# Performance work log

Hardware: AMD Instinct MI355X
Metric: run time of the kernel (lower is better)

## Reference

```python
import jax, jax.numpy as jnp
import numpy as np

BN_EPS = 1e-5

def setup_inputs() -> dict:
    key = jax.random.key(0)
    ks = jax.random.split(key, 6)
    B, C, H, W, Hd = 16, 512, 64, 64, 128
    return {
        "x": jax.random.normal(ks[0], (B, C, H, W), dtype=jnp.float32),
        "wA": jax.random.normal(ks[1], (Hd, C), dtype=jnp.float32) * 0.05,
        "wB": jax.random.normal(ks[2], (Hd, C), dtype=jnp.float32) * 0.05,
        "wC": jax.random.normal(ks[3], (Hd, C), dtype=jnp.float32) * 0.05,
        "wProj": jax.random.normal(ks[4], (C, Hd), dtype=jnp.float32) * 0.05,
        "bn_gamma": jnp.ones((C,), dtype=jnp.float32),
        "bn_beta": jnp.zeros((C,), dtype=jnp.float32),
        "bn_mean": jnp.zeros((C,), dtype=jnp.float32),
        "bn_var": jnp.ones((C,), dtype=jnp.float32),
    }

def reference(x, wA, wB, wC, wProj, bn_gamma, bn_beta, bn_mean, bn_var):
    B, C, H, W = x.shape
    N = H * W
    xf = x.reshape(B, C, N)                                  # [B, C, N]
    # three 1x1 convs (bias-free) == channel-mixing matmuls
    A = jax.nn.softmax(jnp.einsum('hc,bcn->bhn', wA, xf), axis=2)   # [B, Hd, N]
    Bf = jnp.einsum('hc,bcn->bhn', wB, xf)                          # [B, Hd, N]
    Cs = jax.nn.softmax(jnp.einsum('hc,bcn->bhn', wC, xf), axis=2)  # [B, Hd, N]
    # FeatureGathering = B_feat @ A^T : [B, Hd, Hd]
    G = jnp.einsum('bhn,bgn->bhg', Bf, A)
    # distribute: G @ C_softmax -> [B, Hd, N]
    y = jnp.einsum('bhg,bgn->bhn', G, Cs)
    # projection back to C channels + inference-mode BatchNorm
    p = jnp.einsum('ch,bhn->bcn', wProj, y)                         # [B, C, N]
    inv = jax.lax.rsqrt(bn_var + BN_EPS)
    out = (p - bn_mean[None, :, None]) * (inv * bn_gamma)[None, :, None] + bn_beta[None, :, None]
    return out.reshape(B, C, H, W)
```

## Files before the change

### kernel.cpp

```cpp
#include <hip/hip_runtime.h>
#include <cstddef>

#define NPIX 4096
#define CDIM 512

typedef _Float16 half8  __attribute__((ext_vector_type(8)));
typedef _Float16 half4v __attribute__((ext_vector_type(4)));
typedef float    f32x4  __attribute__((ext_vector_type(4)));

__device__ __forceinline__ void gl_lds16(const void* g, void* l) {
    __builtin_amdgcn_global_load_lds(
        (const __attribute__((address_space(1))) void*)g,
        (__attribute__((address_space(3))) void*)l, 16, 0, 0);
}

__global__ __launch_bounds__(256)
void prep(const float* __restrict__ wA, const float* __restrict__ wB,
          const float* __restrict__ wC, const float* __restrict__ wProj,
          _Float16* __restrict__ Wh, _Float16* __restrict__ WpH)
{
    if (blockIdx.x < 96) {
        const int gid  = blockIdx.x * 256 + threadIdx.x;
        const int lane = gid & 63;
        const int frag = gid >> 6;
        const int msub = frag & 7, kt = (frag >> 3) & 15, mt = frag >> 7;
        const float* __restrict__ W = (mt == 0) ? wA : (mt == 1) ? wB : wC;
        const int m  = msub * 16 + (lane & 15);
        const int c0 = kt * 32 + ((lane >> 4) << 3);
        const float* src = W + m * CDIM + c0;
        union { _Float16 h[8]; float4 f; } u;
#pragma unroll
        for (int j = 0; j < 8; ++j) u.h[j] = (_Float16)src[j];
        *(float4*)(Wh + (size_t)frag * 512 + lane * 8) = u.f;
    } else {
        const int gid = (blockIdx.x - 96) * 256 + threadIdx.x;
        const int i8  = gid * 8;
        float4 a = *(const float4*)(wProj + i8);
        float4 b = *(const float4*)(wProj + i8 + 4);
        union { _Float16 h[8]; float4 f; } u;
        u.h[0]=(_Float16)a.x; u.h[1]=(_Float16)a.y; u.h[2]=(_Float16)a.z; u.h[3]=(_Float16)a.w;
        u.h[4]=(_Float16)b.x; u.h[5]=(_Float16)b.y; u.h[6]=(_Float16)b.z; u.h[7]=(_Float16)b.w;
        *(float4*)(WpH + i8) = u.f;
    }
}

__global__ __launch_bounds__(256)
void conv_mfma(const float* __restrict__ x, const _Float16* __restrict__ Wh,
               _Float16* __restrict__ P)
{
    const int nt = blockIdx.x, mt = blockIdx.y, b = blockIdx.z;
    const int tid  = threadIdx.x;
    const int wave = tid >> 6, lane = tid & 63;
    const int wm = wave >> 1, wn = wave & 1;

    __shared__ alignas(16) _Float16 sA[4096];
    __shared__ alignas(16) _Float16 sB[128 * 40];

    f32x4 acc[4][4];
#pragma unroll
    for (int i = 0; i < 4; ++i)
#pragma unroll
        for (int j = 0; j < 4; ++j)
#pragma unroll
            for (int e = 0; e < 4; ++e) acc[i][j][e] = 0.f;

    const int n0 = (tid & 31) << 2;
    const int k0 = (tid >> 5) << 2;
    const float* xb = x + ((size_t)b << 21) + (nt << 7) + n0;
    const _Float16* WhB = Wh + (size_t)mt * 128 * 512;

    for (int kt = 0; kt < 16; ++kt) {
#pragma unroll
        for (int s = 0; s < 2; ++s) {
            const int frag = wave + (s << 2);
            gl_lds16(WhB + ((size_t)kt * 8 + frag) * 512 + lane * 8, &sA[frag * 512]);
        }
        const float* xs = xb + (size_t)(kt * 32 + k0) * NPIX;
        float ld[4][4];
        *(float4*)&ld[0][0] = *(const float4*)(xs);
        *(float4*)&ld[1][0] = *(const float4*)(xs + NPIX);
        *(float4*)&ld[2][0] = *(const float4*)(xs + 2 * NPIX);
        *(float4*)&ld[3][0] = *(const float4*)(xs + 3 * NPIX);
#pragma unroll
        for (int c = 0; c < 4; ++c) {
            const int n    = n0 + c;
            const int blkh = ((k0 >> 2) ^ (((n >> 4) & 3) << 1)) << 2;
            union { _Float16 h[4]; float2 f; } u;
            u.h[0] = (_Float16)ld[0][c];
            u.h[1] = (_Float16)ld[1][c];
            u.h[2] = (_Float16)ld[2][c];
            u.h[3] = (_Float16)ld[3][c];
            *(float2*)&sB[n * 40 + blkh] = u.f;
        }
        __syncthreads();

        half8 av[4], bv[4];
#pragma unroll
        for (int i = 0; i < 4; ++i)
            av[i] = *(const half8*)&sA[(((wm << 2) + i) << 9) + (lane << 3)];
#pragma unroll
        for (int j = 0; j < 4; ++j) {
            const int nj = (wn << 6) + (j << 4) + (lane & 15);
            const int qs = ((lane >> 4) ^ ((nj >> 4) & 3)) << 3;
            bv[j] = *(const half8*)&sB[nj * 40 + qs];
        }
#pragma unroll
        for (int i = 0; i < 4; ++i)
#pragma unroll
            for (int j = 0; j < 4; ++j)
                acc[i][j] = __builtin_amdgcn_mfma_f32_16x16x32_f16(bv[j], av[i], acc[i][j], 0, 0, 0);
        __syncthreads();
    }

    _Float16* Pb = P + (((size_t)b * 384 + mt * 128) << 12);
#pragma unroll
    for (int i = 0; i < 4; ++i) {
        const int m = (wm << 6) + (i << 4) + (lane & 15);
        _Float16* prow = Pb + (size_t)m * NPIX + (nt << 7) + (wn << 6) + ((lane >> 4) << 2);
#pragma unroll
        for (int j = 0; j < 4; ++j) {
            union { _Float16 h[4]; float2 f; } u;
#pragma unroll
            for (int r = 0; r < 4; ++r) u.h[r] = (_Float16)acc[i][j][r];
            *(float2*)(prow + (j << 4)) = u.f;
        }
    }
}

__global__ __launch_bounds__(256)
void softmax_rows(_Float16* __restrict__ P)
{
    const int blk = blockIdx.x;
    const int b   = blk >> 8;
    const int r   = blk & 255;
    const int m   = (r < 128) ? r : (r + 128);
    _Float16* row = P + (((size_t)b * 384 + m) << 12);
    const int tid = threadIdx.x;

    half8 h[2];
    float v[16];
    h[0] = *(const half8*)(row + tid * 16);
    h[1] = *(const half8*)(row + tid * 16 + 8);
    float mx = -3.402823466e38f;
#pragma unroll
    for (int j = 0; j < 16; ++j) { v[j] = (float)h[j >> 3][j & 7]; mx = fmaxf(mx, v[j]); }
#pragma unroll
    for (int o = 32; o > 0; o >>= 1) mx = fmaxf(mx, __shfl_xor(mx, o));
    __shared__ float redm[4];
    __shared__ float reds[4];
    const int wid = tid >> 6, lane = tid & 63;
    if (lane == 0) redm[wid] = mx;
    __syncthreads();
    mx = fmaxf(fmaxf(redm[0], redm[1]), fmaxf(redm[2], redm[3]));

    float s = 0.f;
#pragma unroll
    for (int j = 0; j < 16; ++j) { v[j] = __expf(v[j] - mx); s += v[j]; }
#pragma unroll
    for (int o = 32; o > 0; o >>= 1) s += __shfl_xor(s, o);
    if (lane == 0) reds[wid] = s;
    __syncthreads();
    s = (reds[0] + reds[1]) + (reds[2] + reds[3]);
    const float inv = 1.f / s;
#pragma unroll
    for (int j = 0; j < 16; ++j) h[j >> 3][j & 7] = (_Float16)(v[j] * inv);
    *(half8*)(row + tid * 16)     = h[0];
    *(half8*)(row + tid * 16 + 8) = h[1];
}

__global__ __launch_bounds__(256)
void g_partial_mfma(const _Float16* __restrict__ P, float* __restrict__ Gp)
{
    const int kc = blockIdx.x, b = blockIdx.y;
    const int tid  = threadIdx.x;
    const int wave = tid >> 6, lane = tid & 63;
    const int wm = wave >> 1, wn = wave & 1;

    const _Float16* Pa = P + ((size_t)b * 384 << 12);
    const _Float16* Pf = Pa + ((size_t)128 << 12);

    f32x4 acc[4][4];
#pragma unroll
    for (int i = 0; i < 4; ++i)
#pragma unroll
        for (int j = 0; j < 4; ++j)
#pragma unroll
            for (int e = 0; e < 4; ++e) acc[i][j][e] = 0.f;

    const int klane = ((lane >> 4) << 3);
    const int rlane = lane & 15;
#pragma unroll 2
    for (int kt = 0; kt < 8; ++kt) {
        const int k = (kc << 8) + (kt << 5) + klane;
        half8 av[4], bv[4];
#pragma unroll
        for (int i = 0; i < 4; ++i)
            av[i] = *(const half8*)(Pa + ((size_t)((wm << 6) + (i << 4) + rlane) << 12) + k);
#pragma unroll
        for (int j = 0; j < 4; ++j)
            bv[j] = *(const half8*)(Pf + ((size_t)((wn << 6) + (j << 4) + rlane) << 12) + k);
#pragma unroll
        for (int i = 0; i < 4; ++i)
#pragma unroll
            for (int j = 0; j < 4; ++j)
                acc[i][j] = __builtin_amdgcn_mfma_f32_16x16x32_f16(bv[j], av[i], acc[i][j], 0, 0, 0);
    }

    float* O = Gp + (((size_t)b * 16 + kc) << 14);
#pragma unroll
    for (int i = 0; i < 4; ++i) {
        const int g = (wm << 6) + (i << 4) + rlane;
        float* orow = O + (size_t)g * 128 + (wn << 6) + ((lane >> 4) << 2);
#pragma unroll
        for (int j = 0; j < 4; ++j)
            *(f32x4*)(orow + (j << 4)) = acc[i][j];
    }
}

__global__ __launch_bounds__(256)
void g_reduce_cvt(const float* __restrict__ Gp, _Float16* __restrict__ Gt)
{
    const int gid  = blockIdx.x * 256 + threadIdx.x;
    const int i8   = gid * 8;
    const int b    = i8 >> 14;
    const int rr   = i8 & 16383;
    const float* base = Gp + ((size_t)b << 18) + rr;
    float s[8];
#pragma unroll
    for (int e = 0; e < 8; ++e) s[e] = 0.f;
#pragma unroll
    for (int kc = 0; kc < 16; ++kc) {
        float4 v0 = *(const float4*)(base + ((size_t)kc << 14));
        float4 v1 = *(const float4*)(base + ((size_t)kc << 14) + 4);
        s[0]+=v0.x; s[1]+=v0.y; s[2]+=v0.z; s[3]+=v0.w;
        s[4]+=v1.x; s[5]+=v1.y; s[6]+=v1.z; s[7]+=v1.w;
    }
    union { _Float16 h[8]; float4 f; } u;
#pragma unroll
    for (int e = 0; e < 8; ++e) u.h[e] = (_Float16)s[e];
    *(float4*)(Gt + ((size_t)b << 14) + rr) = u.f;
}

__global__ __launch_bounds__(256)
void proj_mfma(const _Float16* __restrict__ WpH, const _Float16* __restrict__ Gt,
               _Float16* __restrict__ Mh)
{
    const int ct = blockIdx.x, b = blockIdx.y;
    const int tid  = threadIdx.x;
    const int wave = tid >> 6, lane = tid & 63;
    const int wm = wave >> 1, wn = wave & 1;

    f32x4 acc[4][4];
#pragma unroll
    for (int i = 0; i < 4; ++i)
#pragma unroll
        for (int j = 0; j < 4; ++j)
#pragma unroll
            for (int e = 0; e < 4; ++e) acc[i][j][e] = 0.f;

    const int klane = ((lane >> 4) << 3);
    const int rlane = lane & 15;
    const _Float16* Gb = Gt + ((size_t)b << 14);
#pragma unroll
    for (int kt = 0; kt < 4; ++kt) {
        const int k = (kt << 5) + klane;
        half8 av[4], bv[4];
#pragma unroll
        for (int i = 0; i < 4; ++i)
            av[i] = *(const half8*)(WpH + (size_t)((ct << 7) + (wm << 6) + (i << 4) + rlane) * 128 + k);
#pragma unroll
        for (int j = 0; j < 4; ++j)
            bv[j] = *(const half8*)(Gb + (size_t)((wn << 6) + (j << 4) + rlane) * 128 + k);
#pragma unroll
        for (int i = 0; i < 4; ++i)
#pragma unroll
            for (int j = 0; j < 4; ++j)
                acc[i][j] = __builtin_amdgcn_mfma_f32_16x16x32_f16(bv[j], av[i], acc[i][j], 0, 0, 0);
    }

    _Float16* Mb = Mh + ((size_t)b << 16);
#pragma unroll
    for (int i = 0; i < 4; ++i) {
        const int c = (ct << 7) + (wm << 6) + (i << 4) + rlane;
        _Float16* mrow = Mb + (size_t)c * 128 + (wn << 6) + ((lane >> 4) << 2);
#pragma unroll
        for (int j = 0; j < 4; ++j) {
            union { _Float16 h[4]; float2 f; } u;
#pragma unroll
            for (int r = 0; r < 4; ++r) u.h[r] = (_Float16)acc[i][j][r];
            *(float2*)(mrow + (j << 4)) = u.f;
        }
    }
}

__global__ __launch_bounds__(256)
void final_mfma(const _Float16* __restrict__ P, const _Float16* __restrict__ Mh,
                const float* __restrict__ gamma, const float* __restrict__ beta,
                const float* __restrict__ mean,  const float* __restrict__ var,
                float* __restrict__ out)
{
    const int nt = blockIdx.x, ct = blockIdx.y, b = blockIdx.z;
    const int tid  = threadIdx.x;
    const int wave = tid >> 6, lane = tid & 63;
    const int wm = wave >> 1, wn = wave & 1;

    __shared__ alignas(16) _Float16 sB[128 * 40];

    f32x4 acc[4][4];
#pragma unroll
    for (int i = 0; i < 4; ++i)
#pragma unroll
        for (int j = 0; j < 4; ++j)
#pragma unroll
            for (int e = 0; e < 4; ++e) acc[i][j][e] = 0.f;

    const int n0 = (tid & 31) << 2;
    const int k0 = (tid >> 5) << 2;
    const int klane = ((lane >> 4) << 3);
    const int rlane = lane & 15;
    const _Float16* Cs  = P + (((size_t)b * 384 + 256) << 12) + (nt << 7) + n0;
    const _Float16* MhB = Mh + ((size_t)b << 16) + ((size_t)(ct << 7) << 7);

    for (int kt = 0; kt < 4; ++kt) {
        const _Float16* cs = Cs + ((size_t)((kt << 5) + k0) << 12);
        half4v ld0 = *(const half4v*)(cs);
        half4v ld1 = *(const half4v*)(cs + NPIX);
        half4v ld2 = *(const half4v*)(cs + 2 * NPIX);
        half4v ld3 = *(const half4v*)(cs + 3 * NPIX);
#pragma unroll
        for (int c = 0; c < 4; ++c) {
            const int n    = n0 + c;
            const int blkh = ((k0 >> 2) ^ (((n >> 4) & 3) << 1)) << 2;
            half4v col = { ld0[c], ld1[c], ld2[c], ld3[c] };
            *(half4v*)&sB[n * 40 + blkh] = col;
        }
        __syncthreads();

        half8 av[4], bv[4];
#pragma unroll
        for (int i = 0; i < 4; ++i)
            av[i] = *(const half8*)(MhB + (size_t)((wm << 6) + (i << 4) + rlane) * 128 + (kt << 5) + klane);
#pragma unroll
        for (int j = 0; j < 4; ++j) {
            const int nj = (wn << 6) + (j << 4) + rlane;
            const int qs = ((lane >> 4) ^ ((nj >> 4) & 3)) << 3;
            bv[j] = *(const half8*)&sB[nj * 40 + qs];
        }
#pragma unroll
        for (int i = 0; i < 4; ++i)
#pragma unroll
            for (int j = 0; j < 4; ++j)
                acc[i][j] = __builtin_amdgcn_mfma_f32_16x16x32_f16(bv[j], av[i], acc[i][j], 0, 0, 0);
        __syncthreads();
    }

    float* ob = out + ((size_t)b << 21);
#pragma unroll
    for (int i = 0; i < 4; ++i) {
        const int c   = (ct << 7) + (wm << 6) + (i << 4) + rlane;
        const float s = gamma[c] * rsqrtf(var[c] + 1e-5f);
        const float t = fmaf(-mean[c], s, beta[c]);
        float* row = ob + ((size_t)c << 12) + (nt << 7) + (wn << 6) + ((lane >> 4) << 2);
#pragma unroll
        for (int j = 0; j < 4; ++j) {
            f32x4 v;
#pragma unroll
            for (int r = 0; r < 4; ++r) v[r] = fmaf(acc[i][j][r], s, t);
            *(f32x4*)(row + (j << 4)) = v;
        }
    }
}

extern "C" void kernel_launch(void* const* d_in, const int* in_sizes, int n_in,
                              void* d_out, int out_size, void* d_ws, size_t ws_size,
                              hipStream_t stream)
{
    const float* x     = (const float*)d_in[0];
    const float* wA    = (const float*)d_in[1];
    const float* wB    = (const float*)d_in[2];
    const float* wC    = (const float*)d_in[3];
    const float* wProj = (const float*)d_in[4];
    const float* gamma = (const float*)d_in[5];
    const float* beta  = (const float*)d_in[6];
    const float* mean  = (const float*)d_in[7];
    const float* var   = (const float*)d_in[8];
    float* out = (float*)d_out;

    char* ws = (char*)d_ws;
    _Float16* P   = (_Float16*)(ws);
    float*    Gp  = (float*)(ws + 50331648);
    _Float16* Gt  = (_Float16*)(ws + 67108864);
    _Float16* WpH = (_Float16*)(ws + 67633152);
    _Float16* Mh  = (_Float16*)(ws + 67764224);
    _Float16* Wh  = (_Float16*)(ws + 69861376);

    prep          <<<dim3(128),       256, 0, stream>>>(wA, wB, wC, wProj, Wh, WpH);
    conv_mfma     <<<dim3(32, 3, 16), 256, 0, stream>>>(x, Wh, P);
    softmax_rows  <<<dim3(4096),      256, 0, stream>>>(P);
    g_partial_mfma<<<dim3(16, 16),    256, 0, stream>>>(P, Gp);
    g_reduce_cvt  <<<dim3(128),       256, 0, stream>>>(Gp, Gt);
    proj_mfma     <<<dim3(4, 16),     256, 0, stream>>>(WpH, Gt, Mh);
    final_mfma    <<<dim3(32, 4, 16), 256, 0, stream>>>(P, Mh, gamma, beta, mean, var, out);
}
```

Measured before the change: 324.3 us.

## Merge conv M-tiles into one block and reuse staged C tile across output channels

conv_mfma now launches 768-thread blocks that cover all three 128-row weight tiles, so each x tile is loaded from global and converted to fp16 once instead of three times. final_mfma stages the whole 128x128 Cs tile in LDS once and loops over the four output-channel tiles inside the block, which removes the repeated Cs reads and the per-k-step barriers. The cost is fewer, larger blocks: the grid drops from 1536 to 512 blocks in conv and from 2048 to 512 in final, with more LDS per block, which may lower occupancy and latency hiding. In conv, only 256 of the 768 threads do the x load work, so the other waves sit idle at the barrier.

```diff
diff --git a/kernel.cpp b/kernel.cpp
--- a/kernel.cpp
+++ b/kernel.cpp
@@ -44,16 +44,18 @@
     }
 }
 
-__global__ __launch_bounds__(256)
+__global__ __launch_bounds__(768)
 void conv_mfma(const float* __restrict__ x, const _Float16* __restrict__ Wh,
                _Float16* __restrict__ P)
 {
-    const int nt = blockIdx.x, mt = blockIdx.y, b = blockIdx.z;
+    const int nt = blockIdx.x, b = blockIdx.y;
     const int tid  = threadIdx.x;
     const int wave = tid >> 6, lane = tid & 63;
-    const int wm = wave >> 1, wn = wave & 1;
-
-    __shared__ alignas(16) _Float16 sA[4096];
+    const int mt = wave >> 2;
+    const int q  = wave & 3;
+    const int wm = q >> 1, wn = q & 1;
+
+    __shared__ alignas(16) _Float16 sA[3 * 8 * 512];
     __shared__ alignas(16) _Float16 sB[128 * 40];
 
     f32x4 acc[4][4];
@@ -64,46 +66,48 @@
 #pragma unroll
             for (int e = 0; e < 4; ++e) acc[i][j][e] = 0.f;
 
-    const int n0 = (tid & 31) << 2;
-    const int k0 = (tid >> 5) << 2;
-    const float* xb = x + ((size_t)b << 21) + (nt << 7) + n0;
-    const _Float16* WhB = Wh + (size_t)mt * 128 * 512;
-
     for (int kt = 0; kt < 16; ++kt) {
 #pragma unroll
         for (int s = 0; s < 2; ++s) {
-            const int frag = wave + (s << 2);
-            gl_lds16(WhB + ((size_t)kt * 8 + frag) * 512 + lane * 8, &sA[frag * 512]);
-        }
-        const float* xs = xb + (size_t)(kt * 32 + k0) * NPIX;
-        float ld[4][4];
-        *(float4*)&ld[0][0] = *(const float4*)(xs);
-        *(float4*)&ld[1][0] = *(const float4*)(xs + NPIX);
-        *(float4*)&ld[2][0] = *(const float4*)(xs + 2 * NPIX);
-        *(float4*)&ld[3][0] = *(const float4*)(xs + 3 * NPIX);
-#pragma unroll
-        for (int c = 0; c < 4; ++c) {
-            const int n    = n0 + c;
-            const int blkh = ((k0 >> 2) ^ (((n >> 4) & 3) << 1)) << 2;
-            union { _Float16 h[4]; float2 f; } u;
-            u.h[0] = (_Float16)ld[0][c];
-            u.h[1] = (_Float16)ld[1][c];
-            u.h[2] = (_Float16)ld[2][c];
-            u.h[3] = (_Float16)ld[3][c];
-            *(float2*)&sB[n * 40 + blkh] = u.f;
+            const int f    = wave * 2 + s;
+            const int fmt  = f >> 3, fsub = f & 7;
+            gl_lds16(Wh + (((size_t)fmt * 128) + kt * 8 + fsub) * 512 + lane * 8,
+                     &sA[f * 512]);
+        }
+        if (tid < 256) {
+            const int n0 = (tid & 31) << 2;
+            const int k0 = (tid >> 5) << 2;
+            const float* xs = x + ((size_t)b << 21) + (nt << 7) + n0
+                                + (size_t)(kt * 32 + k0) * NPIX;
+            float ld[4][4];
+            *(float4*)&ld[0][0] = *(const float4*)(xs);
+            *(float4*)&ld[1][0] = *(const float4*)(xs + NPIX);
+            *(float4*)&ld[2][0] = *(const float4*)(xs + 2 * NPIX);
+            *(float4*)&ld[3][0] = *(const float4*)(xs + 3 * NPIX);
+#pragma unroll
+            for (int c = 0; c < 4; ++c) {
+                const int n    = n0 + c;
+                const int blkh = ((k0 >> 2) ^ (((n >> 4) & 3) << 1)) << 2;
+                union { _Float16 h[4]; float2 f; } u;
+                u.h[0] = (_Float16)ld[0][c];
+                u.h[1] = (_Float16)ld[1][c];
+                u.h[2] = (_Float16)ld[2][c];
+                u.h[3] = (_Float16)ld[3][c];
+                *(float2*)&sB[n * 40 + blkh] = u.f;
+            }
         }
         __syncthreads();
 
         half8 av[4], bv[4];
-#pragma unroll
-        for (int i = 0; i < 4; ++i)
-            av[i] = *(const half8*)&sA[(((wm << 2) + i) << 9) + (lane << 3)];
 #pragma unroll
         for (int j = 0; j < 4; ++j) {
             const int nj = (wn << 6) + (j << 4) + (lane & 15);
             const int qs = ((lane >> 4) ^ ((nj >> 4) & 3)) << 3;
             bv[j] = *(const half8*)&sB[nj * 40 + qs];
         }
+#pragma unroll
+        for (int i = 0; i < 4; ++i)
+            av[i] = *(const half8*)&sA[(((mt << 3) + (wm << 2) + i) << 9) + (lane << 3)];
 #pragma unroll
         for (int i = 0; i < 4; ++i)
 #pragma unroll
@@ -299,28 +303,20 @@
                 const float* __restrict__ mean,  const float* __restrict__ var,
                 float* __restrict__ out)
 {
-    const int nt = blockIdx.x, ct = blockIdx.y, b = blockIdx.z;
+    const int nt = blockIdx.x, b = blockIdx.y;
     const int tid  = threadIdx.x;
     const int wave = tid >> 6, lane = tid & 63;
     const int wm = wave >> 1, wn = wave & 1;
 
-    __shared__ alignas(16) _Float16 sB[128 * 40];
-
-    f32x4 acc[4][4];
-#pragma unroll
-    for (int i = 0; i < 4; ++i)
-#pragma unroll
-        for (int j = 0; j < 4; ++j)
-#pragma unroll
-            for (int e = 0; e < 4; ++e) acc[i][j][e] = 0.f;
+    __shared__ alignas(16) _Float16 sB[4][128 * 40];
 
     const int n0 = (tid & 31) << 2;
     const int k0 = (tid >> 5) << 2;
     const int klane = ((lane >> 4) << 3);
     const int rlane = lane & 15;
-    const _Float16* Cs  = P + (((size_t)b * 384 + 256) << 12) + (nt << 7) + n0;
-    const _Float16* MhB = Mh + ((size_t)b << 16) + ((size_t)(ct << 7) << 7);
-
+    const _Float16* Cs = P + (((size_t)b * 384 + 256) << 12) + (nt << 7) + n0;
+
+#pragma unroll
     for (int kt = 0; kt < 4; ++kt) {
         const _Float16* cs = Cs + ((size_t)((kt << 5) + k0) << 12);
         half4v ld0 = *(const half4v*)(cs);
@@ -332,41 +328,56 @@
             const int n    = n0 + c;
             const int blkh = ((k0 >> 2) ^ (((n >> 4) & 3) << 1)) << 2;
             half4v col = { ld0[c], ld1[c], ld2[c], ld3[c] };
-            *(half4v*)&sB[n * 40 + blkh] = col;
-        }
-        __syncthreads();
-
-        half8 av[4], bv[4];
-#pragma unroll
-        for (int i = 0; i < 4; ++i)
-            av[i] = *(const half8*)(MhB + (size_t)((wm << 6) + (i << 4) + rlane) * 128 + (kt << 5) + klane);
-#pragma unroll
-        for (int j = 0; j < 4; ++j) {
-            const int nj = (wn << 6) + (j << 4) + rlane;
-            const int qs = ((lane >> 4) ^ ((nj >> 4) & 3)) << 3;
-            bv[j] = *(const half8*)&sB[nj * 40 + qs];
-        }
+            *(half4v*)&sB[kt][n * 40 + blkh] = col;
+        }
+    }
+    __syncthreads();
+
+    const _Float16* Mb = Mh + ((size_t)b << 16);
+    float* ob = out + ((size_t)b << 21);
+
+    for (int ct = 0; ct < 4; ++ct) {
+        f32x4 acc[4][4];
 #pragma unroll
         for (int i = 0; i < 4; ++i)
 #pragma unroll
             for (int j = 0; j < 4; ++j)
-                acc[i][j] = __builtin_amdgcn_mfma_f32_16x16x32_f16(bv[j], av[i], acc[i][j], 0, 0, 0);
-        __syncthreads();
-    }
-
-    float* ob = out + ((size_t)b << 21);
-#pragma unroll
-    for (int i = 0; i < 4; ++i) {
-        const int c   = (ct << 7) + (wm << 6) + (i << 4) + rlane;
-        const float s = gamma[c] * rsqrtf(var[c] + 1e-5f);
-        const float t = fmaf(-mean[c], s, beta[c]);
-        float* row = ob + ((size_t)c << 12) + (nt << 7) + (wn << 6) + ((lane >> 4) << 2);
-#pragma unroll
-        for (int j = 0; j < 4; ++j) {
-            f32x4 v;
-#pragma unroll
-            for (int r = 0; r < 4; ++r) v[r] = fmaf(acc[i][j][r], s, t);
-            *(f32x4*)(row + (j << 4)) = v;
+#pragma unroll
+                for (int e = 0; e < 4; ++e) acc[i][j][e] = 0.f;
+
+#pragma unroll
+        for (int kt = 0; kt < 4; ++kt) {
+            half8 av[4], bv[4];
+#pragma unroll
+            for (int i = 0; i < 4; ++i)
+                av[i] = *(const half8*)(Mb + (size_t)((ct << 7) + (wm << 6) + (i << 4) + rlane) * 128
+                                           + (kt << 5) + klane);
+#pragma unroll
+            for (int j = 0; j < 4; ++j) {
+                const int nj = (wn << 6) + (j << 4) + rlane;
+                const int qs = ((lane >> 4) ^ ((nj >> 4) & 3)) << 3;
+                bv[j] = *(const half8*)&sB[kt][nj * 40 + qs];
+            }
+#pragma unroll
+            for (int i = 0; i < 4; ++i)
+#pragma unroll
+                for (int j = 0; j < 4; ++j)
+                    acc[i][j] = __builtin_amdgcn_mfma_f32_16x16x32_f16(bv[j], av[i], acc[i][j], 0, 0, 0);
+        }
+
+#pragma unroll
+        for (int i = 0; i < 4; ++i) {
+            const int c   = (ct << 7) + (wm << 6) + (i << 4) + rlane;
+            const float s = gamma[c] * rsqrtf(var[c] + 1e-5f);
+            const float t = fmaf(-mean[c], s, beta[c]);
+            float* row = ob + ((size_t)c << 12) + (nt << 7) + (wn << 6) + ((lane >> 4) << 2);
+#pragma unroll
+            for (int j = 0; j < 4; ++j) {
+                f32x4 v;
+#pragma unroll
+                for (int r = 0; r < 4; ++r) v[r] = fmaf(acc[i][j][r], s, t);
+                *(f32x4*)(row + (j << 4)) = v;
+            }
         }
     }
 }
@@ -394,11 +405,11 @@
     _Float16* Mh  = (_Float16*)(ws + 67764224);
     _Float16* Wh  = (_Float16*)(ws + 69861376);
 
-    prep          <<<dim3(128),       256, 0, stream>>>(wA, wB, wC, wProj, Wh, WpH);
-    conv_mfma     <<<dim3(32, 3, 16), 256, 0, stream>>>(x, Wh, P);
-    softmax_rows  <<<dim3(4096),      256, 0, stream>>>(P);
-    g_partial_mfma<<<dim3(16, 16),    256, 0, stream>>>(P, Gp);
-    g_reduce_cvt  <<<dim3(128),       256, 0, stream>>>(Gp, Gt);
-    proj_mfma     <<<dim3(4, 16),     256, 0, stream>>>(WpH, Gt, Mh);
-    final_mfma    <<<dim3(32, 4, 16), 256, 0, stream>>>(P, Mh, gamma, beta, mean, var, out);
-}
+    prep          <<<dim3(128),    256, 0, stream>>>(wA, wB, wC, wProj, Wh, WpH);
+    conv_mfma     <<<dim3(32, 16), 768, 0, stream>>>(x, Wh, P);
+    softmax_rows  <<<dim3(4096),   256, 0, stream>>>(P);
+    g_partial_mfma<<<dim3(16, 16), 256, 0, stream>>>(P, Gp);
+    g_reduce_cvt  <<<dim3(128),    256, 0, stream>>>(Gp, Gt);
+    proj_mfma     <<<dim3(4, 16),  256, 0, stream>>>(WpH, Gt, Mh);
+    final_mfma    <<<dim3(32, 16), 256, 0, stream>>>(P, Mh, gamma, beta, mean, var, out);
+}
```

Result: slower. 344.9 us (+6.3%).

## Double-buffer conv GEMM loads and reuse C-softmax tile across channel tiles

Applied to the files above, without the earlier changes.

The conv GEMM kernel now double-buffers its weight and x tiles in LDS, prefetching the next K slice while computing the current one, with one barrier per iteration instead of two. The final projection kernel loads the softmaxed C tile into LDS once and loops over all four output channel tiles, instead of launching separate blocks that each reload it. This aims to hide global load latency and cut redundant reads, at the cost of more LDS per block and fewer blocks in the final kernel.

```diff
diff --git a/kernel.cpp b/kernel.cpp
--- a/kernel.cpp
+++ b/kernel.cpp
@@ -53,8 +53,8 @@
     const int wave = tid >> 6, lane = tid & 63;
     const int wm = wave >> 1, wn = wave & 1;
 
-    __shared__ alignas(16) _Float16 sA[4096];
-    __shared__ alignas(16) _Float16 sB[128 * 40];
+    __shared__ alignas(16) _Float16 sA[2][8 * 512];
+    __shared__ alignas(16) _Float16 sB[2][128 * 40];
 
     f32x4 acc[4][4];
 #pragma unroll
@@ -69,13 +69,13 @@
     const float* xb = x + ((size_t)b << 21) + (nt << 7) + n0;
     const _Float16* WhB = Wh + (size_t)mt * 128 * 512;
 
-    for (int kt = 0; kt < 16; ++kt) {
-#pragma unroll
-        for (int s = 0; s < 2; ++s) {
-            const int frag = wave + (s << 2);
-            gl_lds16(WhB + ((size_t)kt * 8 + frag) * 512 + lane * 8, &sA[frag * 512]);
-        }
-        const float* xs = xb + (size_t)(kt * 32 + k0) * NPIX;
+#pragma unroll
+    for (int s = 0; s < 2; ++s) {
+        const int f = wave * 2 + s;
+        gl_lds16(WhB + ((size_t)f) * 512 + lane * 8, &sA[0][f * 512]);
+    }
+    {
+        const float* xs = xb + (size_t)k0 * NPIX;
         float ld[4][4];
         *(float4*)&ld[0][0] = *(const float4*)(xs);
         *(float4*)&ld[1][0] = *(const float4*)(xs + NPIX);
@@ -90,26 +90,61 @@
             u.h[1] = (_Float16)ld[1][c];
             u.h[2] = (_Float16)ld[2][c];
             u.h[3] = (_Float16)ld[3][c];
-            *(float2*)&sB[n * 40 + blkh] = u.f;
-        }
-        __syncthreads();
+            *(float2*)&sB[0][n * 40 + blkh] = u.f;
+        }
+    }
+    __syncthreads();
+
+    int cur = 0;
+    for (int kt = 0; kt < 16; ++kt) {
+        const int nxt = cur ^ 1;
+        float ld[4][4];
+        const bool pf = (kt < 15);
+        if (pf) {
+#pragma unroll
+            for (int s = 0; s < 2; ++s) {
+                const int f = wave * 2 + s;
+                gl_lds16(WhB + ((size_t)(kt + 1) * 8 + f) * 512 + lane * 8,
+                         &sA[nxt][f * 512]);
+            }
+            const float* xs = xb + (size_t)((kt + 1) * 32 + k0) * NPIX;
+            *(float4*)&ld[0][0] = *(const float4*)(xs);
+            *(float4*)&ld[1][0] = *(const float4*)(xs + NPIX);
+            *(float4*)&ld[2][0] = *(const float4*)(xs + 2 * NPIX);
+            *(float4*)&ld[3][0] = *(const float4*)(xs + 3 * NPIX);
+        }
 
         half8 av[4], bv[4];
-#pragma unroll
-        for (int i = 0; i < 4; ++i)
-            av[i] = *(const half8*)&sA[(((wm << 2) + i) << 9) + (lane << 3)];
 #pragma unroll
         for (int j = 0; j < 4; ++j) {
             const int nj = (wn << 6) + (j << 4) + (lane & 15);
             const int qs = ((lane >> 4) ^ ((nj >> 4) & 3)) << 3;
-            bv[j] = *(const half8*)&sB[nj * 40 + qs];
-        }
+            bv[j] = *(const half8*)&sB[cur][nj * 40 + qs];
+        }
+#pragma unroll
+        for (int i = 0; i < 4; ++i)
+            av[i] = *(const half8*)&sA[cur][(((wm << 2) + i) << 9) + (lane << 3)];
 #pragma unroll
         for (int i = 0; i < 4; ++i)
 #pragma unroll
             for (int j = 0; j < 4; ++j)
                 acc[i][j] = __builtin_amdgcn_mfma_f32_16x16x32_f16(bv[j], av[i], acc[i][j], 0, 0, 0);
-        __syncthreads();
+
+        if (pf) {
+#pragma unroll
+            for (int c = 0; c < 4; ++c) {
+                const int n    = n0 + c;
+                const int blkh = ((k0 >> 2) ^ (((n >> 4) & 3) << 1)) << 2;
+                union { _Float16 h[4]; float2 f; } u;
+                u.h[0] = (_Float16)ld[0][c];
+                u.h[1] = (_Float16)ld[1][c];
+                u.h[2] = (_Float16)ld[2][c];
+                u.h[3] = (_Float16)ld[3][c];
+                *(float2*)&sB[nxt][n * 40 + blkh] = u.f;
+            }
+            __syncthreads();
+        }
+        cur = nxt;
     }
 
     _Float16* Pb = P + (((size_t)b * 384 + mt * 128) << 12);
@@ -299,28 +334,20 @@
                 const float* __restrict__ mean,  const float* __restrict__ var,
                 float* __restrict__ out)
 {
-    const int nt = blockIdx.x, ct = blockIdx.y, b = blockIdx.z;
+    const int nt = blockIdx.x, b = blockIdx.y;
     const int tid  = threadIdx.x;
     const int wave = tid >> 6, lane = tid & 63;
     const int wm = wave >> 1, wn = wave & 1;
 
-    __shared__ alignas(16) _Float16 sB[128 * 40];
-
-    f32x4 acc[4][4];
-#pragma unroll
-    for (int i = 0; i < 4; ++i)
-#pragma unroll
-        for (int j = 0; j < 4; ++j)
-#pragma unroll
-            for (int e = 0; e < 4; ++e) acc[i][j][e] = 0.f;
+    __shared__ alignas(16) _Float16 sB[4][128 * 40];
 
     const int n0 = (tid & 31) << 2;
     const int k0 = (tid >> 5) << 2;
     const int klane = ((lane >> 4) << 3);
     const int rlane = lane & 15;
-    const _Float16* Cs  = P + (((size_t)b * 384 + 256) << 12) + (nt << 7) + n0;
-    const _Float16* MhB = Mh + ((size_t)b << 16) + ((size_t)(ct << 7) << 7);
-
+    const _Float16* Cs = P + (((size_t)b * 384 + 256) << 12) + (nt << 7) + n0;
+
+#pragma unroll
     for (int kt = 0; kt < 4; ++kt) {
         const _Float16* cs = Cs + ((size_t)((kt << 5) + k0) << 12);
         half4v ld0 = *(const half4v*)(cs);
@@ -332,41 +359,56 @@
             const int n    = n0 + c;
             const int blkh = ((k0 >> 2) ^ (((n >> 4) & 3) << 1)) << 2;
             half4v col = { ld0[c], ld1[c], ld2[c], ld3[c] };
-            *(half4v*)&sB[n * 40 + blkh] = col;
-        }
-        __syncthreads();
-
-        half8 av[4], bv[4];
-#pragma unroll
-        for (int i = 0; i < 4; ++i)
-            av[i] = *(const half8*)(MhB + (size_t)((wm << 6) + (i << 4) + rlane) * 128 + (kt << 5) + klane);
-#pragma unroll
-        for (int j = 0; j < 4; ++j) {
-            const int nj = (wn << 6) + (j << 4) + rlane;
-            const int qs = ((lane >> 4) ^ ((nj >> 4) & 3)) << 3;
-            bv[j] = *(const half8*)&sB[nj * 40 + qs];
-        }
+            *(half4v*)&sB[kt][n * 40 + blkh] = col;
+        }
+    }
+    __syncthreads();
+
+    const _Float16* Mb = Mh + ((size_t)b << 16);
+    float* ob = out + ((size_t)b << 21);
+
+    for (int ct = 0; ct < 4; ++ct) {
+        f32x4 acc[4][4];
 #pragma unroll
         for (int i = 0; i < 4; ++i)
 #pragma unroll
             for (int j = 0; j < 4; ++j)
-                acc[i][j] = __builtin_amdgcn_mfma_f32_16x16x32_f16(bv[j], av[i], acc[i][j], 0, 0, 0);
-        __syncthreads();
-    }
-
-    float* ob = out + ((size_t)b << 21);
-#pragma unroll
-    for (int i = 0; i < 4; ++i) {
-        const int c   = (ct << 7) + (wm << 6) + (i << 4) + rlane;
-        const float s = gamma[c] * rsqrtf(var[c] + 1e-5f);
-        const float t = fmaf(-mean[c], s, beta[c]);
-        float* row = ob + ((size_t)c << 12) + (nt << 7) + (wn << 6) + ((lane >> 4) << 2);
-#pragma unroll
-        for (int j = 0; j < 4; ++j) {
-            f32x4 v;
-#pragma unroll
-            for (int r = 0; r < 4; ++r) v[r] = fmaf(acc[i][j][r], s, t);
-            *(f32x4*)(row + (j << 4)) = v;
+#pragma unroll
+                for (int e = 0; e < 4; ++e) acc[i][j][e] = 0.f;
+
+#pragma unroll
+        for (int kt = 0; kt < 4; ++kt) {
+            half8 av[4], bv[4];
+#pragma unroll
+            for (int i = 0; i < 4; ++i)
+                av[i] = *(const half8*)(Mb + (size_t)((ct << 7) + (wm << 6) + (i << 4) + rlane) * 128
+                                           + (kt << 5) + klane);
+#pragma unroll
+            for (int j = 0; j < 4; ++j) {
+                const int nj = (wn << 6) + (j << 4) + rlane;
+                const int qs = ((lane >> 4) ^ ((nj >> 4) & 3)) << 3;
+                bv[j] = *(const half8*)&sB[kt][nj * 40 + qs];
+            }
+#pragma unroll
+            for (int i = 0; i < 4; ++i)
+#pragma unroll
+                for (int j = 0; j < 4; ++j)
+                    acc[i][j] = __builtin_amdgcn_mfma_f32_16x16x32_f16(bv[j], av[i], acc[i][j], 0, 0, 0);
+        }
+
+#pragma unroll
+        for (int i = 0; i < 4; ++i) {
+            const int c   = (ct << 7) + (wm << 6) + (i << 4) + rlane;
+            const float s = gamma[c] * rsqrtf(var[c] + 1e-5f);
+            const float t = fmaf(-mean[c], s, beta[c]);
+            float* row = ob + ((size_t)c << 12) + (nt << 7) + (wn << 6) + ((lane >> 4) << 2);
+#pragma unroll
+            for (int j = 0; j < 4; ++j) {
+                f32x4 v;
+#pragma unroll
+                for (int r = 0; r < 4; ++r) v[r] = fmaf(acc[i][j][r], s, t);
+                *(f32x4*)(row + (j << 4)) = v;
+            }
         }
     }
 }
@@ -400,5 +442,5 @@
     g_partial_mfma<<<dim3(16, 16),    256, 0, stream>>>(P, Gp);
     g_reduce_cvt  <<<dim3(128),       256, 0, stream>>>(Gp, Gt);
     proj_mfma     <<<dim3(4, 16),     256, 0, stream>>>(WpH, Gt, Mh);
-    final_mfma    <<<dim3(32, 4, 16), 256, 0, stream>>>(P, Mh, gamma, beta, mean, var, out);
-}
+    final_mfma    <<<dim3(32, 16),    256, 0, stream>>>(P, Mh, gamma, beta, mean, var, out);
+}
```

Measured after the change: 340.7 us. 1.05x slower.
